# Kernel optimization log

Measured on AMD Instinct MI355X. Metric: run time of the kernel, lower is better.

## Reference

```python
import jax, jax.numpy as jnp
import numpy as np
from jax import lax

B, S, T, H, VIN, VOUT = 32, 128, 64, 512, 32000, 32000
PAD_IDX = 1


def setup_inputs() -> dict:
    key = jax.random.key(0)
    ks = jax.random.split(key, 20)
    sc = 0.05
    rn = lambda k, shp: (jax.random.normal(k, shp, jnp.float32) * sc)
    return {
        "src": jax.random.randint(ks[0], (B, S), 0, VIN),
        "src_len": jnp.full((B,), S, dtype=jnp.int32),
        "trg": jax.random.randint(ks[1], (B, T), 0, VOUT),
        "enc_emb": rn(ks[2], (VIN, H)),
        "enc_wih": rn(ks[3], (4 * H, H)),
        "enc_whh": rn(ks[4], (4 * H, H)),
        "enc_bih": rn(ks[5], (4 * H,)),
        "enc_bhh": rn(ks[6], (4 * H,)),
        "enc_fc_w": rn(ks[7], (H, H)),
        "enc_fc_b": rn(ks[8], (H,)),
        "dec_emb": rn(ks[9], (VOUT, H)),
        "attn_w": rn(ks[10], (H, 2 * H)),
        "attn_b": rn(ks[11], (H,)),
        "attn_v": rn(ks[12], (H,)),
        "dec_wih": rn(ks[13], (4 * H, 2 * H)),
        "dec_whh": rn(ks[14], (4 * H, H)),
        "dec_bih": rn(ks[15], (4 * H,)),
        "dec_bhh": rn(ks[16], (4 * H,)),
        "out_w": rn(ks[17], (VOUT, 3 * H)),
        "out_b": rn(ks[18], (VOUT,)),
    }


def _lstm_cell(x, h, c, wih, whh, bih, bhh):
    # PyTorch gate order: i, f, g, o
    g = x @ wih.T + bih + h @ whh.T + bhh
    i, f, gg, o = jnp.split(g, 4, axis=-1)
    c = jax.nn.sigmoid(f) * c + jax.nn.sigmoid(i) * jnp.tanh(gg)
    h = jax.nn.sigmoid(o) * jnp.tanh(c)
    return h, c


def reference(src, src_len, trg, enc_emb, enc_wih, enc_whh, enc_bih, enc_bhh,
              enc_fc_w, enc_fc_b, dec_emb, attn_w, attn_b, attn_v,
              dec_wih, dec_whh, dec_bih, dec_bhh, out_w, out_b):
    b = src.shape[0]
    # ---- Encoder: single-layer LSTM over time (full lengths) ----
    emb = enc_emb[src].transpose(1, 0, 2)  # [S,B,H] time-major
    h0 = jnp.zeros((b, H), emb.dtype)
    c0 = jnp.zeros((b, H), emb.dtype)

    def enc_step(carry, x_t):
        h, c = carry
        h, c = _lstm_cell(x_t, h, c, enc_wih, enc_whh, enc_bih, enc_bhh)
        return (h, c), h

    (hf, cf), enc_out = lax.scan(enc_step, (h0, c0), emb)  # enc_out [S,B,H]
    hidden = jnp.tanh(hf @ enc_fc_w.T + enc_fc_b)  # [B,H]
    enc_bt = enc_out.transpose(1, 0, 2)  # [B,S,H]
    mask = src != PAD_IDX  # [B,S]

    # ---- Decoder: teacher forcing (ratio=1.0), scan over target steps ----
    def dec_step(carry, tok):
        h, c = carry
        e = dec_emb[tok]  # [B,H]
        # Bahdanau attention
        hrep = jnp.broadcast_to(h[:, None, :], enc_bt.shape)  # [B,S,H]
        energy = jnp.tanh(jnp.concatenate([hrep, enc_bt], -1) @ attn_w.T + attn_b)
        score = energy @ attn_v  # [B,S]
        score = jnp.where(mask, score, jnp.float32(-1e10))
        a = jax.nn.softmax(score, axis=1)
        weighted = jnp.einsum('bs,bsh->bh', a, enc_bt)  # [B,H]
        x = jnp.concatenate([e, weighted], -1)  # [B,2H]
        h, c = _lstm_cell(x, h, c, dec_wih, dec_whh, dec_bih, dec_bhh)
        pred = jnp.concatenate([h, weighted, e], -1) @ out_w.T + out_b  # [B,V]
        return (h, c), pred

    tokens = trg.T  # [T,B]
    (_, _), logits = lax.scan(dec_step, (hidden, cf), tokens[:-1])  # [T-1,B,V]
    outputs = jnp.concatenate(
        [jnp.zeros((1, b, VOUT), logits.dtype), logits], axis=0)  # [T,B,V]
    return outputs
```

## Files before the change

kernel.cpp:

```cpp
#include <hip/hip_runtime.h>

typedef unsigned short u16;
typedef unsigned int u32;
typedef unsigned long long u64;
typedef __attribute__((ext_vector_type(8))) short bf16x8;
typedef __attribute__((ext_vector_type(8))) unsigned short u16x8;
typedef __attribute__((ext_vector_type(4))) unsigned short u16x4;
typedef __attribute__((ext_vector_type(4))) float f32x4;

#define DEVI static __device__ __forceinline__
#define MFMA __builtin_amdgcn_mfma_f32_16x16x32_bf16

constexpr int B = 32, S = 128, T = 64, H = 512, V = 32000;
constexpr int H4 = 4 * H;
constexpr int TD = T - 1;
constexpr int MOUT = TD * B;
constexpr int KOUT = 3 * H;
constexpr int PAD_IDX = 1;

DEVI u16 f2bf(float f) {
  union { float f; unsigned u; } v; v.f = f;
  unsigned r = (v.u + 0x7fffu + ((v.u >> 16) & 1u)) >> 16;
  return (u16)r;
}
DEVI float bf2f(u16 h) {
  union { unsigned u; float f; } v; v.u = ((unsigned)h) << 16;
  return v.f;
}
DEVI float sigm(float x) { return 1.f / (1.f + __expf(-x)); }
DEVI float tanh_(float x) {
  float ax = fabsf(x);
  float e = __expf(-2.f * ax);
  float t = (1.f - e) / (1.f + e);
  return x < 0.f ? -t : t;
}
DEVI float tanhf_(float x) {
  float e = __expf(2.f * x);
  return 1.f - 2.f * __builtin_amdgcn_rcpf(e + 1.f);
}
DEVI int swz(int row, int k8) { return row * 32 + ((k8 ^ (row & 3)) << 3); }

DEVI u64 pack4u(const u16* p) {
  return (u64)p[0] | ((u64)p[1] << 16) | ((u64)p[2] << 32) | ((u64)p[3] << 48);
}
DEVI u64 xstore(u16* p, u64 v) {
  return __hip_atomic_exchange((u64*)p, v, __ATOMIC_RELAXED,
                               __HIP_MEMORY_SCOPE_AGENT);
}
DEVI void sstore(unsigned* p, unsigned v) {
  __hip_atomic_exchange(p, v, __ATOMIC_RELAXED, __HIP_MEMORY_SCOPE_AGENT);
}
DEVI void poll_bo(unsigned* p, unsigned tgt) {
  int it = 0;
  long long t0 = (long long)__builtin_amdgcn_s_memrealtime();
  while (__hip_atomic_load(p, __ATOMIC_RELAXED, __HIP_MEMORY_SCOPE_AGENT) <
         tgt) {
    if (it < 4) {
      __builtin_amdgcn_s_sleep(1);
      it++;
    } else {
      __builtin_amdgcn_s_sleep(8);
    }
    if ((long long)__builtin_amdgcn_s_memrealtime() - t0 > 20000000ll) break;
  }
}

__global__ __launch_bounds__(256) void gemm_bt(
    const u16* __restrict__ A, int lda,
    const u16* __restrict__ Bt, int ldb,
    float* __restrict__ C, int ldc,
    const float* __restrict__ bias, int M, int K, int bf16out) {
  __shared__ u16 As[128 * 32], Bs[128 * 32];
  const int tid = threadIdx.x;
  const int m0 = blockIdx.y * 128, n0 = blockIdx.x * 128;
  const int lane = tid & 63, w = tid >> 6, wm = w >> 1, wn = w & 1;
  const int lr = lane & 15, lk = lane >> 4;
  f32x4 acc[4][4] = {};
  const int r = tid >> 1, cc = (tid & 1) * 16, k8b = (tid & 1) * 2;

  for (int k0 = 0; k0 < K; k0 += 32) {
    {
      long gr = m0 + r;
      u16x8 v0 = {}, v1 = {};
      if (gr < M) {
        const u16* s = A + gr * (long)lda + k0 + cc;
        v0 = *(const u16x8*)s;
        v1 = *(const u16x8*)(s + 8);
      }
      *(u16x8*)&As[swz(r, k8b)] = v0;
      *(u16x8*)&As[swz(r, k8b + 1)] = v1;
    }
    {
      const u16* s = Bt + (long)(n0 + r) * ldb + k0 + cc;
      u16x8 v0 = *(const u16x8*)s;
      u16x8 v1 = *(const u16x8*)(s + 8);
      *(u16x8*)&Bs[swz(r, k8b)] = v0;
      *(u16x8*)&Bs[swz(r, k8b + 1)] = v1;
    }
    __syncthreads();
    bf16x8 af[4], bfr[4];
#pragma unroll
    for (int mi = 0; mi < 4; mi++)
      af[mi] = *(const bf16x8*)&As[swz(wm * 64 + mi * 16 + lr, lk)];
#pragma unroll
    for (int ni = 0; ni < 4; ni++)
      bfr[ni] = *(const bf16x8*)&Bs[swz(wn * 64 + ni * 16 + lr, lk)];
#pragma unroll
    for (int mi = 0; mi < 4; mi++)
#pragma unroll
      for (int ni = 0; ni < 4; ni++)
        acc[mi][ni] = MFMA(af[mi], bfr[ni], acc[mi][ni], 0, 0, 0);
    __syncthreads();
  }
#pragma unroll
  for (int ni = 0; ni < 4; ni++) {
    int col = n0 + wn * 64 + ni * 16 + lr;
    float bs = bias ? bias[col] : 0.f;
#pragma unroll
    for (int mi = 0; mi < 4; mi++) {
#pragma unroll
      for (int rr = 0; rr < 4; rr++) {
        long row = m0 + wm * 64 + mi * 16 + lk * 4 + rr;
        if (row < M) {
          float v = acc[mi][ni][rr] + bs;
          if (bf16out)
            ((u16*)C)[row * (long)ldc + col] = f2bf(v);
          else
            C[row * (long)ldc + col] = v;
        }
      }
    }
  }
}

__global__ void zero_f(float* p, long n) {
  long i = (long)blockIdx.x * 256 + threadIdx.x;
  long st = (long)gridDim.x * 256;
  for (; i < n; i += st) p[i] = 0.f;
}

__global__ void zero_u(unsigned* p, int n) {
  int i = blockIdx.x * 256 + threadIdx.x;
  if (i < n) p[i] = 0u;
}

__global__ void cast_bf(const float* __restrict__ src, u16* __restrict__ dst,
                        int ld, int off, int Csz) {
  long row = blockIdx.y;
  int col = blockIdx.x * 256 + threadIdx.x;
  dst[row * Csz + col] = f2bf(src[row * ld + off + col]);
}

__global__ void cast_bf4(const float* __restrict__ src, u16* __restrict__ dst,
                         long n4) {
  long i = (long)blockIdx.x * 256 + threadIdx.x;
  if (i >= n4) return;
  float4 v = ((const float4*)src)[i];
  u16x4 o;
  o[0] = f2bf(v.x); o[1] = f2bf(v.y); o[2] = f2bf(v.z); o[3] = f2bf(v.w);
  *(u16x4*)&dst[i * 4] = o;
}

__global__ void cast_perm(const float* __restrict__ src, int ld, int off,
                          u16* __restrict__ dst) {
  int np = blockIdx.y;
  int c = blockIdx.x * 256 + threadIdx.x;
  int g = np & 3, jH = np >> 2;
  dst[(size_t)np * H + c] = f2bf(src[(size_t)(g * H + jH) * ld + off + c]);
}

__global__ void pack_wdec_p(const float* __restrict__ wih,
                            const float* __restrict__ whh,
                            u16* __restrict__ dst) {
  int r = blockIdx.y;
  int k = blockIdx.x * 256 + threadIdx.x;
  int g = r & 3, j = r >> 2;
  int srow = g * H + j;
  float v = (k < 512) ? wih[(size_t)srow * (2 * H) + 512 + k]
                      : whh[(size_t)srow * H + (k - 512)];
  dst[(size_t)r * 1024 + k] = f2bf(v);
}

__global__ void bias_perm(const float* __restrict__ a,
                          const float* __restrict__ b, float* __restrict__ o) {
  int np = blockIdx.x * 256 + threadIdx.x;
  int g = np & 3, jH = np >> 2;
  int r = g * H + jH;
  o[np] = a[r] + b[r];
}

__global__ __launch_bounds__(256) void cast_transpose_bf(
    const float* __restrict__ src, int ld, int off, u16* __restrict__ dst,
    int R) {
  __shared__ float tile[32][33];
  int r0 = blockIdx.y * 32, c0 = blockIdx.x * 32;
  int tx = threadIdx.x & 31, ty = threadIdx.x >> 5;
#pragma unroll
  for (int i = 0; i < 32; i += 8)
    tile[ty + i][tx] = src[(long)(r0 + ty + i) * ld + off + c0 + tx];
  __syncthreads();
#pragma unroll
  for (int i = 0; i < 32; i += 8)
    dst[(long)(c0 + ty + i) * R + r0 + tx] = f2bf(tile[tx][ty + i]);
}

__global__ void gather_src_emb(const int* __restrict__ src,
                               const float* __restrict__ emb,
                               u16* __restrict__ dst) {
  int row = blockIdx.y;
  int t = row >> 5, b = row & 31;
  int c = blockIdx.x * 256 + threadIdx.x;
  int tok = src[b * S + t];
  dst[(long)row * H + c] = f2bf(emb[(long)tok * H + c]);
}

__global__ void gather_trg_emb(const int* __restrict__ trg,
                               const float* __restrict__ emb,
                               u16* __restrict__ xout) {
  int row = blockIdx.y;
  int t = row >> 5, b = row & 31;
  int c = blockIdx.x * 256 + threadIdx.x;
  int tok = trg[b * T + t];
  xout[(long)row * KOUT + 2 * H + c] = f2bf(emb[(long)tok * H + c]);
}

__global__ __launch_bounds__(512) void enc_persist32(
    unsigned* fes, const u16* __restrict__ wenc_p,
    const float* __restrict__ xih_p, u16* hstep, u16* enc_bt_bf, float* cbuf) {
  __shared__ float gs[32][64];
  __shared__ float c_s[512];
  __shared__ u16 hx[512];
  const int tid = threadIdx.x, bk = blockIdx.x;
  const int wave = tid >> 6, lane = tid & 63;
  const int lr = lane & 15, lk = lane >> 4;
  const int bq = tid >> 4, jl = tid & 15;
  c_s[tid] = 0.f;
  const int mt = wave & 1, nt = wave >> 1;
  const int n = nt * 16 + lr;
  const u16* wp = wenc_p + (size_t)(bk * 64 + n) * 512 + lk * 8;
  for (int t = 0; t < S; t++) {
    if (t > 0 && tid < 32) poll_bo(fes + tid * 16, (unsigned)t);
    __syncthreads();
    float4 xv = *(const float4*)(xih_p + ((size_t)t * B + bq) * H4 +
                                 (bk * 16 + jl) * 4);
    {
      const u16* ab =
          hstep + (size_t)t * B * H + (size_t)(mt * 16 + lr) * H + lk * 8;
      f32x4 acc = {};
#pragma unroll
      for (int kt = 0; kt < 16; kt++) {
        bf16x8 a = *(const bf16x8*)(ab + kt * 32);
        bf16x8 w = *(const bf16x8*)(wp + kt * 32);
        acc = MFMA(a, w, acc, 0, 0, 0);
      }
#pragma unroll
      for (int rr = 0; rr < 4; rr++) gs[mt * 16 + lk * 4 + rr][n] = acc[rr];
    }
    __syncthreads();
    {
      float gi = xv.x + gs[bq][jl * 4 + 0];
      float gf = xv.y + gs[bq][jl * 4 + 1];
      float gg = xv.z + gs[bq][jl * 4 + 2];
      float go = xv.w + gs[bq][jl * 4 + 3];
      float cn = sigm(gf) * c_s[tid] + sigm(gi) * tanh_(gg);
      c_s[tid] = cn;
      u16 h16 = f2bf(sigm(go) * tanh_(cn));
      hx[tid] = h16;
      enc_bt_bf[((size_t)bq * S + t) * H + bk * 16 + jl] = h16;
    }
    __syncthreads();
    u64 kp = 0;
    if (tid < 128) {
      int bb = tid >> 2, q = tid & 3;
      kp = xstore(hstep + (size_t)(t + 1) * B * H + (size_t)bb * H + bk * 16 +
                      q * 4,
                  pack4u(&hx[bb * 16 + q * 4]));
    }
    if (wave < 2) {
      asm volatile("" :: "v"(kp));
      asm volatile("s_waitcnt vmcnt(0)" ::: "memory");
    }
    __syncthreads();
    if (tid == 0) sstore(fes + bk * 16, (unsigned)(t + 1));
  }
  cbuf[bq * H + bk * 16 + jl] = c_s[tid];
}

__global__ __launch_bounds__(512) void dec_persist32(
    unsigned* fhs, unsigned* fws, const float* __restrict__ fc_w,
    const float* __restrict__ fc_b, const u16* __restrict__ wdec_p,
    const u16* __restrict__ a1T_bf, const float* __restrict__ attn_v,
    const int* __restrict__ src, const u16* __restrict__ hf_bf,
    const float* __restrict__ cbuf, const u16* __restrict__ epart_bf,
    const u16* __restrict__ enc_bt_bf, const float* __restrict__ eih_p,
    u16* hstep, u16* wstep, u16* __restrict__ xout_bf) {
  __shared__ float buf[8][512];
  __shared__ float hs[512], hps[512];
  __shared__ float sc[128], red[2];
  __shared__ int smask[128];
  __shared__ float c_s[512];
  __shared__ u16 hx[512];
  const int tid = threadIdx.x, bk = blockIdx.x;
  const int wave = tid >> 6, lane = tid & 63;
  const int lr = lane & 15, lk = lane >> 4;
  const int bq = tid >> 4, jl = tid & 15;
  c_s[tid] = cbuf[bq * H + bk * 16 + jl];
  if (tid < 128) smask[tid] = src[bk * S + tid];
  float av8[8];
#pragma unroll
  for (int e = 0; e < 8; e++) av8[e] = attn_v[lane * 8 + e];
  if (wave < 2) {
    const u16* ab = hf_bf + (size_t)(wave * 16 + lr) * H + lk * 8;
    const float* frow = fc_w + (size_t)(bk * 16 + lr) * H + lk * 8;
    f32x4 acc = {};
#pragma unroll
    for (int kt = 0; kt < 16; kt++) {
      bf16x8 a = *(const bf16x8*)(ab + kt * 32);
      bf16x8 w;
#pragma unroll
      for (int e = 0; e < 8; e++) w[e] = (short)f2bf(frow[kt * 32 + e]);
      acc = MFMA(a, w, acc, 0, 0, 0);
    }
    float bs = fc_b[bk * 16 + lr];
#pragma unroll
    for (int rr = 0; rr < 4; rr++)
      hx[(wave * 16 + lk * 4 + rr) * 16 + lr] = f2bf(tanh_(acc[rr] + bs));
  }
  __syncthreads();
  {
    u64 kp = 0;
    if (tid < 128) {
      int bb = tid >> 2, q = tid & 3;
      kp = xstore(hstep + (size_t)bb * H + bk * 16 + q * 4,
                  pack4u(&hx[bb * 16 + q * 4]));
    }
    if (wave < 2) {
      asm volatile("" :: "v"(kp));
      asm volatile("s_waitcnt vmcnt(0)" ::: "memory");
    }
    __syncthreads();
    if (tid == 0) sstore(fhs + bk * 16, 1u);
  }
  const int mt = wave & 1, nt = wave >> 1;
  const int n = nt * 16 + lr;
  const u16* wpw = wdec_p + (size_t)(bk * 64 + n) * 1024 + lk * 8;
  const u16* wph = wpw + 512;
  for (int t = 0; t < TD; t++) {
    if (tid < 32) poll_bo(fhs + tid * 16, (unsigned)(t + 1));
    __syncthreads();
    float4 xv = *(const float4*)(eih_p + ((size_t)t * B + bq) * H4 +
                                 (bk * 16 + jl) * 4);
    if (tid < 256) {
      u32 v = ((const u32*)(hstep + (size_t)t * B * H + (size_t)bk * H))[tid];
      hs[2 * tid] = bf2f((u16)(v & 0xffff));
      hs[2 * tid + 1] = bf2f((u16)(v >> 16));
    }
    __syncthreads();
    {
      float p[8] = {};
      const int j0 = lane * 8;
#pragma unroll 4
      for (int kk = 0; kk < 64; kk++) {
        int k = wave * 64 + kk;
        float hk = hs[k];
        u16x8 av = *(const u16x8*)&a1T_bf[(size_t)k * H + j0];
#pragma unroll
        for (int e = 0; e < 8; e++) p[e] += hk * bf2f(av[e]);
      }
#pragma unroll
      for (int e = 0; e < 8; e++) buf[wave][j0 + e] = p[e];
    }
    __syncthreads();
    {
      float s0 = 0.f;
#pragma unroll
      for (int w = 0; w < 8; w++) s0 += buf[w][tid];
      hps[tid] = s0;
    }
    __syncthreads();
    {
      const int j0 = lane * 8;
      float hp8[8];
#pragma unroll
      for (int e = 0; e < 8; e++) hp8[e] = hps[j0 + e];
      for (int i = 0; i < 16; i++) {
        int s = wave * 16 + i;
        u16x8 ep = *(const u16x8*)&epart_bf[((size_t)bk * S + s) * H + j0];
        float a = 0.f;
#pragma unroll
        for (int e = 0; e < 8; e++) a += av8[e] * tanhf_(hp8[e] + bf2f(ep[e]));
#pragma unroll
        for (int o = 32; o; o >>= 1) a += __shfl_xor(a, o);
        if (lane == 0) sc[s] = (smask[s] == PAD_IDX) ? -1e10f : a;
      }
    }
    __syncthreads();
    if (tid < 64) {
      float v = fmaxf(sc[tid], sc[tid + 64]);
#pragma unroll
      for (int o = 32; o; o >>= 1) v = fmaxf(v, __shfl_xor(v, o));
      if (tid == 0) red[0] = v;
    }
    __syncthreads();
    float mx = red[0];
    if (tid < S) sc[tid] = __expf(sc[tid] - mx);
    __syncthreads();
    if (tid < 64) {
      float v = sc[tid] + sc[tid + 64];
#pragma unroll
      for (int o = 32; o; o >>= 1) v += __shfl_xor(v, o);
      if (tid == 0) red[1] = 1.f / v;
    }
    __syncthreads();
    {
      float acc8[8] = {};
      const int j0 = lane * 8;
      for (int i = 0; i < 16; i++) {
        int s = wave * 16 + i;
        float ps = sc[s];
        u16x8 ev = *(const u16x8*)&enc_bt_bf[((size_t)bk * S + s) * H + j0];
#pragma unroll
        for (int e = 0; e < 8; e++) acc8[e] += ps * bf2f(ev[e]);
      }
#pragma unroll
      for (int e = 0; e < 8; e++) buf[wave][j0 + e] = acc8[e];
    }
    __syncthreads();
    {
      u64 kp = 0;
      if (tid < 128) {
        float inv = red[1];
        int j0 = tid * 4;
        u16x4 o;
#pragma unroll
        for (int i = 0; i < 4; i++) {
          float wj = (buf[0][j0 + i] + buf[1][j0 + i] + buf[2][j0 + i] +
                      buf[3][j0 + i] + buf[4][j0 + i] + buf[5][j0 + i] +
                      buf[6][j0 + i] + buf[7][j0 + i]) *
                     inv;
          o[i] = f2bf(wj);
        }
        *(u16x4*)&xout_bf[((size_t)t * B + bk) * KOUT + H + j0] = o;
        u64 val = (u64)o[0] | ((u64)o[1] << 16) | ((u64)o[2] << 32) |
                  ((u64)o[3] << 48);
        kp = xstore(wstep + ((size_t)t * B + bk) * H + j0, val);
      }
      if (wave < 2) {
        asm volatile("" :: "v"(kp));
        asm volatile("s_waitcnt vmcnt(0)" ::: "memory");
      }
      __syncthreads();
      if (tid == 0) sstore(fws + bk * 16, (unsigned)(t + 1));
    }
    if (tid < 32) poll_bo(fws + tid * 16, (unsigned)(t + 1));
    __syncthreads();
    {
      const u16* aw =
          wstep + (size_t)t * B * H + (size_t)(mt * 16 + lr) * H + lk * 8;
      const u16* ah =
          hstep + (size_t)t * B * H + (size_t)(mt * 16 + lr) * H + lk * 8;
      f32x4 acc = {};
#pragma unroll
      for (int kt = 0; kt < 16; kt++) {
        bf16x8 a = *(const bf16x8*)(aw + kt * 32);
        bf16x8 w = *(const bf16x8*)(wpw + kt * 32);
        acc = MFMA(a, w, acc, 0, 0, 0);
      }
#pragma unroll
      for (int kt = 0; kt < 16; kt++) {
        bf16x8 a = *(const bf16x8*)(ah + kt * 32);
        bf16x8 w = *(const bf16x8*)(wph + kt * 32);
        acc = MFMA(a, w, acc, 0, 0, 0);
      }
      float* gsp = &buf[0][0];
#pragma unroll
      for (int rr = 0; rr < 4; rr++)
        gsp[(mt * 16 + lk * 4 + rr) * 64 + n] = acc[rr];
    }
    __syncthreads();
    {
      const float* gsp = &buf[0][0];
      float gi = xv.x + gsp[bq * 64 + jl * 4 + 0];
      float gf = xv.y + gsp[bq * 64 + jl * 4 + 1];
      float gg = xv.z + gsp[bq * 64 + jl * 4 + 2];
      float go = xv.w + gsp[bq * 64 + jl * 4 + 3];
      float cn = sigm(gf) * c_s[tid] + sigm(gi) * tanh_(gg);
      c_s[tid] = cn;
      u16 h16 = f2bf(sigm(go) * tanh_(cn));
      hx[tid] = h16;
      xout_bf[((size_t)t * B + bq) * KOUT + bk * 16 + jl] = h16;
    }
    __syncthreads();
    {
      u64 kp = 0;
      if (tid < 128) {
        int bb = tid >> 2, q = tid & 3;
        kp = xstore(hstep + (size_t)(t + 1) * B * H + (size_t)bb * H +
                        bk * 16 + q * 4,
                    pack4u(&hx[bb * 16 + q * 4]));
      }
      if (wave < 2) {
        asm volatile("" :: "v"(kp));
        asm volatile("s_waitcnt vmcnt(0)" ::: "memory");
      }
      __syncthreads();
      if (tid == 0) sstore(fhs + bk * 16, (unsigned)(t + 2));
    }
  }
}

extern "C" void kernel_launch(void* const* d_in, const int* in_sizes, int n_in,
                              void* d_out, int out_size, void* d_ws,
                              size_t ws_size, hipStream_t stream) {
  const int* src = (const int*)d_in[0];
  const int* trg = (const int*)d_in[2];
  const float* enc_emb = (const float*)d_in[3];
  const float* enc_wih = (const float*)d_in[4];
  const float* enc_whh = (const float*)d_in[5];
  const float* enc_bih = (const float*)d_in[6];
  const float* enc_bhh = (const float*)d_in[7];
  const float* fc_w = (const float*)d_in[8];
  const float* fc_b = (const float*)d_in[9];
  const float* dec_emb = (const float*)d_in[10];
  const float* attn_w = (const float*)d_in[11];
  const float* attn_b = (const float*)d_in[12];
  const float* attn_v = (const float*)d_in[13];
  const float* dec_wih = (const float*)d_in[14];
  const float* dec_whh = (const float*)d_in[15];
  const float* dec_bih = (const float*)d_in[16];
  const float* dec_bhh = (const float*)d_in[17];
  const float* out_w = (const float*)d_in[18];
  const float* out_b = (const float*)d_in[19];
  float* out = (float*)d_out;

  char* wp = (char*)d_ws;
  auto alloc = [&](size_t n) {
    char* p = wp;
    wp += (n + 255) & ~(size_t)255;
    return p;
  };
  u16* outw_bf = (u16*)alloc((size_t)V * KOUT * 2);
  u16* wihenc_p = (u16*)alloc((size_t)H4 * H * 2);
  u16* wihE_p = (u16*)alloc((size_t)H4 * H * 2);
  u16* wenc_p = (u16*)alloc((size_t)H4 * H * 2);
  u16* wdec_p = (u16*)alloc((size_t)H4 * 2 * H * 2);
  u16* attnw2_bf = (u16*)alloc((size_t)H * H * 2);
  u16* a1T_bf = (u16*)alloc((size_t)H * H * 2);
  u16* xemb_bf = (u16*)alloc((size_t)S * B * H * 2);
  float* xih_p = (float*)alloc((size_t)S * B * H4 * 4);
  u16* enc_bt_bf = (u16*)alloc((size_t)B * S * H * 2);
  u16* epart_bf = (u16*)alloc((size_t)B * S * H * 2);
  float* eih_p = (float*)alloc((size_t)MOUT * H4 * 4);
  u16* xout_bf = (u16*)alloc((size_t)MOUT * KOUT * 2);
  u16* hstep_enc = (u16*)alloc((size_t)(S + 1) * B * H * 2);
  u16* hstep_dec = (u16*)alloc((size_t)T * B * H * 2);
  u16* wstep = (u16*)alloc((size_t)TD * B * H * 2);
  float* cbuf = (float*)alloc((size_t)B * H * 4);
  float* benc_p = (float*)alloc((size_t)H4 * 4);
  float* bdec_p = (float*)alloc((size_t)H4 * 4);
  unsigned* flags = (unsigned*)alloc(2048 * 4);
  unsigned* fes = flags;
  unsigned* fhs = flags + 512;
  unsigned* fws = flags + 1024;

  dim3 blk(256);
  zero_f<<<dim3(256), blk, 0, stream>>>(out, (long)B * V);
  zero_u<<<dim3(8), blk, 0, stream>>>(flags, 2048);
  zero_u<<<dim3(32), blk, 0, stream>>>((unsigned*)hstep_enc, B * H / 2);
  cast_bf4<<<dim3(((long)V * KOUT / 4 + 255) / 256), blk, 0, stream>>>(
      out_w, outw_bf, (long)V * KOUT / 4);
  cast_perm<<<dim3(H / 256, H4), blk, 0, stream>>>(enc_wih, H, 0, wihenc_p);
  cast_perm<<<dim3(H / 256, H4), blk, 0, stream>>>(dec_wih, 2 * H, 0, wihE_p);
  cast_perm<<<dim3(H / 256, H4), blk, 0, stream>>>(enc_whh, H, 0, wenc_p);
  pack_wdec_p<<<dim3(4, H4), blk, 0, stream>>>(dec_wih, dec_whh, wdec_p);
  cast_bf<<<dim3(H / 256, H), blk, 0, stream>>>(attn_w, attnw2_bf, 2 * H, H, H);
  cast_transpose_bf<<<dim3(H / 32, H / 32), blk, 0, stream>>>(attn_w, 2 * H, 0,
                                                              a1T_bf, H);
  bias_perm<<<dim3(H4 / 256), blk, 0, stream>>>(enc_bih, enc_bhh, benc_p);
  bias_perm<<<dim3(H4 / 256), blk, 0, stream>>>(dec_bih, dec_bhh, bdec_p);
  gather_src_emb<<<dim3(H / 256, S * B), blk, 0, stream>>>(src, enc_emb,
                                                           xemb_bf);
  gather_trg_emb<<<dim3(H / 256, MOUT), blk, 0, stream>>>(trg, dec_emb,
                                                          xout_bf);
  gemm_bt<<<dim3(H4 / 128, (S * B) / 128), blk, 0, stream>>>(
      xemb_bf, H, wihenc_p, H, xih_p, H4, benc_p, S * B, H, 0);
  gemm_bt<<<dim3(H4 / 128, (MOUT + 127) / 128), blk, 0, stream>>>(
      xout_bf + 2 * H, KOUT, wihE_p, H, eih_p, H4, bdec_p, MOUT, H, 0);
  enc_persist32<<<dim3(32), dim3(512), 0, stream>>>(fes, wenc_p, xih_p,
                                                    hstep_enc, enc_bt_bf, cbuf);
  gemm_bt<<<dim3(H / 128, (B * S) / 128), blk, 0, stream>>>(
      enc_bt_bf, H, attnw2_bf, H, (float*)epart_bf, H, attn_b, B * S, H, 1);
  dec_persist32<<<dim3(32), dim3(512), 0, stream>>>(
      fhs, fws, fc_w, fc_b, wdec_p, a1T_bf, attn_v, src,
      hstep_enc + (size_t)S * B * H, cbuf, epart_bf, enc_bt_bf, eih_p,
      hstep_dec, wstep, xout_bf);
  gemm_bt<<<dim3(V / 128, (MOUT + 127) / 128), blk, 0, stream>>>(
      xout_bf, KOUT, outw_bf, KOUT, out + (size_t)B * V, V, out_b, MOUT, KOUT,
      0);
}
```

Baseline: 3.265 ms.

## Keep recurrent weights in registers and hoist decoder hidden-state GEMM before attention

```diff
diff --git a/kernel.cpp b/kernel.cpp
--- a/kernel.cpp
+++ b/kernel.cpp
@@ -237,7 +237,12 @@
   c_s[tid] = 0.f;
   const int mt = wave & 1, nt = wave >> 1;
   const int n = nt * 16 + lr;
-  const u16* wp = wenc_p + (size_t)(bk * 64 + n) * 512 + lk * 8;
+  bf16x8 wf[16];
+  {
+    const u16* wp = wenc_p + (size_t)(bk * 64 + n) * 512 + lk * 8;
+#pragma unroll
+    for (int kt = 0; kt < 16; kt++) wf[kt] = *(const bf16x8*)(wp + kt * 32);
+  }
   for (int t = 0; t < S; t++) {
     if (t > 0 && tid < 32) poll_bo(fes + tid * 16, (unsigned)t);
     __syncthreads();
@@ -250,8 +255,7 @@
 #pragma unroll
       for (int kt = 0; kt < 16; kt++) {
         bf16x8 a = *(const bf16x8*)(ab + kt * 32);
-        bf16x8 w = *(const bf16x8*)(wp + kt * 32);
-        acc = MFMA(a, w, acc, 0, 0, 0);
+        acc = MFMA(a, wf[kt], acc, 0, 0, 0);
       }
 #pragma unroll
       for (int rr = 0; rr < 4; rr++) gs[mt * 16 + lk * 4 + rr][n] = acc[rr];
@@ -296,6 +300,8 @@
     u16* hstep, u16* wstep, u16* __restrict__ xout_bf) {
   __shared__ float buf[8][512];
   __shared__ float hs[512], hps[512];
+  __shared__ float gh[32][64];
+  __shared__ float gw[32][64];
   __shared__ float sc[128], red[2];
   __shared__ int smask[128];
   __shared__ float c_s[512];
@@ -345,11 +351,27 @@
   const int n = nt * 16 + lr;
   const u16* wpw = wdec_p + (size_t)(bk * 64 + n) * 1024 + lk * 8;
   const u16* wph = wpw + 512;
+  bf16x8 wwf[16];
+#pragma unroll
+  for (int kt = 0; kt < 16; kt++) wwf[kt] = *(const bf16x8*)(wpw + kt * 32);
   for (int t = 0; t < TD; t++) {
     if (tid < 32) poll_bo(fhs + tid * 16, (unsigned)(t + 1));
     __syncthreads();
     float4 xv = *(const float4*)(eih_p + ((size_t)t * B + bq) * H4 +
                                  (bk * 16 + jl) * 4);
+    {
+      const u16* ah =
+          hstep + (size_t)t * B * H + (size_t)(mt * 16 + lr) * H + lk * 8;
+      f32x4 acc = {};
+#pragma unroll
+      for (int kt = 0; kt < 16; kt++) {
+        bf16x8 a = *(const bf16x8*)(ah + kt * 32);
+        bf16x8 w = *(const bf16x8*)(wph + kt * 32);
+        acc = MFMA(a, w, acc, 0, 0, 0);
+      }
+#pragma unroll
+      for (int rr = 0; rr < 4; rr++) gh[mt * 16 + lk * 4 + rr][n] = acc[rr];
+    }
     if (tid < 256) {
       u32 v = ((const u32*)(hstep + (size_t)t * B * H + (size_t)bk * H))[tid];
       hs[2 * tid] = bf2f((u16)(v & 0xffff));
@@ -359,7 +381,7 @@
     {
       float p[8] = {};
       const int j0 = lane * 8;
-#pragma unroll 4
+#pragma unroll 8
       for (int kk = 0; kk < 64; kk++) {
         int k = wave * 64 + kk;
         float hk = hs[k];
@@ -383,6 +405,7 @@
       float hp8[8];
 #pragma unroll
       for (int e = 0; e < 8; e++) hp8[e] = hps[j0 + e];
+#pragma unroll 4
       for (int i = 0; i < 16; i++) {
         int s = wave * 16 + i;
         u16x8 ep = *(const u16x8*)&epart_bf[((size_t)bk * S + s) * H + j0];
@@ -415,6 +438,7 @@
     {
       float acc8[8] = {};
       const int j0 = lane * 8;
+#pragma unroll 4
       for (int i = 0; i < 16; i++) {
         int s = wave * 16 + i;
         float ps = sc[s];
@@ -457,33 +481,21 @@
     {
       const u16* aw =
           wstep + (size_t)t * B * H + (size_t)(mt * 16 + lr) * H + lk * 8;
-      const u16* ah =
-          hstep + (size_t)t * B * H + (size_t)(mt * 16 + lr) * H + lk * 8;
       f32x4 acc = {};
 #pragma unroll
       for (int kt = 0; kt < 16; kt++) {
         bf16x8 a = *(const bf16x8*)(aw + kt * 32);
-        bf16x8 w = *(const bf16x8*)(wpw + kt * 32);
-        acc = MFMA(a, w, acc, 0, 0, 0);
-      }
-#pragma unroll
-      for (int kt = 0; kt < 16; kt++) {
-        bf16x8 a = *(const bf16x8*)(ah + kt * 32);
-        bf16x8 w = *(const bf16x8*)(wph + kt * 32);
-        acc = MFMA(a, w, acc, 0, 0, 0);
-      }
-      float* gsp = &buf[0][0];
-#pragma unroll
-      for (int rr = 0; rr < 4; rr++)
-        gsp[(mt * 16 + lk * 4 + rr) * 64 + n] = acc[rr];
-    }
-    __syncthreads();
-    {
-      const float* gsp = &buf[0][0];
-      float gi = xv.x + gsp[bq * 64 + jl * 4 + 0];
-      float gf = xv.y + gsp[bq * 64 + jl * 4 + 1];
-      float gg = xv.z + gsp[bq * 64 + jl * 4 + 2];
-      float go = xv.w + gsp[bq * 64 + jl * 4 + 3];
+        acc = MFMA(a, wwf[kt], acc, 0, 0, 0);
+      }
+#pragma unroll
+      for (int rr = 0; rr < 4; rr++) gw[mt * 16 + lk * 4 + rr][n] = acc[rr];
+    }
+    __syncthreads();
+    {
+      float gi = xv.x + gh[bq][jl * 4 + 0] + gw[bq][jl * 4 + 0];
+      float gf = xv.y + gh[bq][jl * 4 + 1] + gw[bq][jl * 4 + 1];
+      float gg = xv.z + gh[bq][jl * 4 + 2] + gw[bq][jl * 4 + 2];
+      float go = xv.w + gh[bq][jl * 4 + 3] + gw[bq][jl * 4 + 3];
       float cn = sigm(gf) * c_s[tid] + sigm(gi) * tanh_(gg);
       c_s[tid] = cn;
       u16 h16 = f2bf(sigm(go) * tanh_(cn));
```

Measured after the change: 3.182 ms. 1.03x faster.
